# Performance work log

Hardware: AMD Instinct MI355X
Metric: run time of the kernel (lower is better)

## Reference

```python
import jax, jax.numpy as jnp
from jax import lax
import numpy as np

K = 7  # deformable conv kernel size
DN = ('NHWC', 'HWIO', 'NHWC')


def pad_zeros_2d(x, f=2):
    # zero-stuffing upsample by factor f in H and W (PadZeros2D(num_zeros=(2,2)))
    B, H, W, C = x.shape
    out = jnp.zeros((B, H * f, W * f, C), x.dtype)
    return out.at[:, ::f, ::f, :].set(x)


def bilinear_sample(x, pos):
    # x: [B,H,W,C]; pos: [B,H,W,KK,2] float (y,x) -> [B,H,W,KK,C]; out-of-bounds -> 0
    B, H, W, C = x.shape
    y, xx = pos[..., 0], pos[..., 1]
    y0 = jnp.floor(y)
    x0 = jnp.floor(xx)
    wy1 = y - y0
    wx1 = xx - x0
    b = jnp.arange(B)[:, None, None, None]

    def gather(yi, xi):
        valid = (yi >= 0) & (yi <= H - 1) & (xi >= 0) & (xi <= W - 1)
        yc = jnp.clip(yi, 0, H - 1).astype(jnp.int32)
        xc = jnp.clip(xi, 0, W - 1).astype(jnp.int32)
        return x[b, yc, xc] * valid[..., None].astype(x.dtype)

    return (gather(y0, x0) * ((1 - wy1) * (1 - wx1))[..., None]
            + gather(y0, x0 + 1) * ((1 - wy1) * wx1)[..., None]
            + gather(y0 + 1, x0) * (wy1 * (1 - wx1))[..., None]
            + gather(y0 + 1, x0 + 1) * (wy1 * wx1)[..., None])


def deform_conv2d(x, off_w, off_b, w, b):
    # deformable conv v1: offsets predicted by a same-padded KxK conv,
    # bilinear sampling at (base + kernel offset + learned offset), then accumulate.
    B, H, W, C = x.shape
    F = w.shape[-1]
    off = lax.conv_general_dilated(x, off_w, (1, 1), 'SAME', dimension_numbers=DN) + off_b
    off = off.reshape(B, H, W, K * K, 2)
    ki, kj = jnp.meshgrid(jnp.arange(K) - K // 2, jnp.arange(K) - K // 2, indexing='ij')
    kpos = jnp.stack([ki.ravel(), kj.ravel()], -1).astype(x.dtype)  # [49,2]
    base = jnp.stack(jnp.meshgrid(jnp.arange(H), jnp.arange(W), indexing='ij'), -1).astype(x.dtype)  # [H,W,2]
    pos = base[None, :, :, None, :] + kpos[None, None, None] + off  # [B,H,W,49,2]
    samp = bilinear_sample(x, pos)  # [B,H,W,49,C]
    return jnp.einsum('bhwkc,kcf->bhwf', samp, w.reshape(K * K, C, F)) + b


def setup_inputs() -> dict:
    key = jax.random.key(0)
    ks = jax.random.split(key, 20)
    latent, in_shape, chan = 128, (8, 16, 1024), 1
    D = int(np.prod(in_shape))
    filt = [in_shape[-1], 64, 32, 16, chan]

    def conv_w(k, cin, cout):
        return jax.random.normal(k, (K, K, cin, cout), jnp.float32) / np.sqrt(K * K * cin)

    inp = {
        'z_in': jax.random.normal(ks[0], (2, latent), jnp.float32),
        'dense_w': jax.random.normal(ks[1], (latent, D), jnp.float32) / np.sqrt(latent),
        'dense_b': jnp.zeros((D,), jnp.float32),
    }
    for i in range(4):
        cin, cout = filt[i], filt[i + 1]
        inp[f'ow{i+1}'] = conv_w(ks[2 + 4 * i], cin, 2 * K * K) * 0.01  # small offsets
        inp[f'ob{i+1}'] = jnp.zeros((2 * K * K,), jnp.float32)
        inp[f'w{i+1}'] = conv_w(ks[3 + 4 * i], cin, cout)
        inp[f'b{i+1}'] = jnp.zeros((cout,), jnp.float32)
    return inp


def reference(z_in, dense_w, dense_b, ow1, ob1, w1, b1, ow2, ob2, w2, b2,
              ow3, ob3, w3, b3, ow4, ob4, w4, b4):
    B = z_in.shape[0]
    x = jax.nn.relu((z_in @ dense_w + dense_b).reshape(B, 8, 16, 1024))
    x = jax.nn.relu(deform_conv2d(pad_zeros_2d(x), ow1, ob1, w1, b1))  # [B,16,32,64]
    x = jax.nn.relu(deform_conv2d(pad_zeros_2d(x), ow2, ob2, w2, b2))  # [B,32,64,32]
    x = jax.nn.relu(deform_conv2d(pad_zeros_2d(x), ow3, ob3, w3, b3))  # [B,64,128,16]
    x = deform_conv2d(pad_zeros_2d(x), ow4, ob4, w4, b4)               # [B,128,256,1]
    return x  # activation is linear
```

## Files before the change

kernel.cpp:

```cpp
#include <hip/hip_runtime.h>
#include <hip/hip_bf16.h>

#define K49 49

typedef short bf16x8 __attribute__((ext_vector_type(8)));
typedef float f32x4 __attribute__((ext_vector_type(4)));

__device__ __forceinline__ short f2bf(float x) {
    __hip_bfloat16 h = __float2bfloat16(x);
    return __builtin_bit_cast(short, h);
}
__device__ __forceinline__ float bf2f(short s) {
    unsigned u = ((unsigned)(unsigned short)s) << 16;
    return __builtin_bit_cast(float, u);
}

__device__ __forceinline__ void d_pack_ow1(
    const int gid, const float* __restrict__ OW, short* __restrict__ OWbf)
{
    const int ni = gid & 15;
    int t = gid >> 4;
    const int kg = t & 3;  t >>= 2;
    const int kb = t & 31; t >>= 5;
    const int nt = t % 7;
    const int d  = t / 7;
    const int oc = nt * 16 + ni;
    short h[8];
    if (oc < 98) {
        const int c0 = kb * 32 + kg * 8;
        #pragma unroll
        for (int j = 0; j < 8; ++j)
            h[j] = f2bf(OW[((size_t)d * 1024 + c0 + j) * 98 + oc]);
    } else {
        #pragma unroll
        for (int j = 0; j < 8; ++j) h[j] = 0;
    }
    *(bf16x8*)(OWbf + (size_t)gid * 8) = *(bf16x8*)h;
}

template<int C, int F>
__device__ __forceinline__ void d_pack_w(
    const int gid, const float* __restrict__ Wt, short* __restrict__ Wf)
{
    constexpr int KB = C / 32;
    constexpr int NT = F / 16;
    constexpr int PLANE = 49 * NT * KB * 4 * 16 * 8;
    const int ni = gid & 15;
    int t = gid >> 4;
    const int kg = t & 3; t >>= 2;
    const int kb = t % KB; t /= KB;
    const int nt = t % NT;
    const int d  = t / NT;
    const int f = nt * 16 + ni;
    const int c0 = kb * 32 + kg * 8;
    short hi[8], lo[8];
    #pragma unroll
    for (int j = 0; j < 8; ++j) {
        const float v = Wt[((size_t)d * C + c0 + j) * F + f];
        hi[j] = f2bf(v);
        lo[j] = f2bf(v - bf2f(hi[j]));
    }
    *(bf16x8*)(Wf + (size_t)gid * 8) = *(bf16x8*)hi;
    *(bf16x8*)(Wf + PLANE + (size_t)gid * 8) = *(bf16x8*)lo;
}

template<int C>
__device__ __forceinline__ void d_pack_owf(
    const int gid, const float* __restrict__ OW, short* __restrict__ OWf)
{
    const int j = gid & 7;
    int t = gid >> 3;
    const int fi = t & 63; t >>= 6;
    const int nt = t % 7;
    const int kbg = t / 7;
    const int ni = fi & 15, kg = fi >> 4;

    int cum1, cum2, cum3;
    if (C == 64)      { cum1 = 18; cum2 = 42; cum3 = 66; }
    else if (C == 32) { cum1 = 9;  cum2 = 21; cum3 = 33; }
    else              { cum1 = 5;  cum2 = 11; cum3 = 17; }
    int cls, kb0;
    if (kbg < cum1)      { cls = 0; kb0 = 0; }
    else if (kbg < cum2) { cls = 1; kb0 = cum1; }
    else if (kbg < cum3) { cls = 2; kb0 = cum2; }
    else                 { cls = 3; kb0 = cum3; }
    const int kbl = kbg - kb0;
    const int pi = cls >> 1, rho = cls & 1;
    const int NRc = pi ? 4 : 3, NCc = rho ? 4 : 3;
    const int T = NRc * NCc;

    const int k = kbl * 32 + kg * 8 + j;
    const int tl = k / C, c = k - tl * C;
    const int oc = nt * 16 + ni;
    float v = 0.f;
    if (tl < T && oc < 98) {
        const int iy = tl / NCc, ix = tl - iy * NCc;
        const int d = (1 - pi + 2 * iy) * 7 + (1 - rho + 2 * ix);
        v = OW[((size_t)d * C + c) * 98 + oc];
    }
    OWf[gid] = f2bf(v);
}

__global__ __launch_bounds__(256) void k_prep(
    const float* __restrict__ z, const float* __restrict__ Wd,
    const float* __restrict__ bd, short* __restrict__ Xf,
    const float* __restrict__ ow1, const float* __restrict__ w1,
    const float* __restrict__ ow2, const float* __restrict__ w2,
    const float* __restrict__ ow3, const float* __restrict__ w3,
    const float* __restrict__ ow4,
    short* OWbf, short* W1f, short* OWf2, short* W2f,
    short* OWf3, short* W3f, short* OWf4)
{
    const int bid0 = blockIdx.x;
    const int tid = threadIdx.x;
    __shared__ float zs[256];
    if (bid0 < 512) {
        const int D = 131072;
        zs[tid] = z[tid];
        __syncthreads();
        const int n = bid0 * 256 + tid;
        const float bb = bd[n];
        float a0 = bb, a1 = bb;
        #pragma unroll 8
        for (int kk = 0; kk < 128; ++kk) {
            const float w = Wd[kk * D + n];
            a0 = fmaf(zs[kk], w, a0);
            a1 = fmaf(zs[128 + kk], w, a1);
        }
        a0 = fmaxf(a0, 0.f);
        a1 = fmaxf(a1, 0.f);
        const int c = n & 1023;
        const int m0 = n >> 10;
        const int kb = c >> 5, kg = (c >> 3) & 3, j = c & 7;
        const size_t base = ((size_t)kb * 4 + kg) * 16 * 8 + j;
        {
            const size_t dst = ((size_t)(m0 >> 4) * 2048) * 8 + base + (size_t)(m0 & 15) * 8;
            const short h = f2bf(a0);
            Xf[dst] = h;
            Xf[262144 + dst] = f2bf(a0 - bf2f(h));
        }
        {
            const int m1 = m0 + 128;
            const size_t dst = ((size_t)(m1 >> 4) * 2048) * 8 + base + (size_t)(m1 & 15) * 8;
            const short h = f2bf(a1);
            Xf[dst] = h;
            Xf[262144 + dst] = f2bf(a1 - bf2f(h));
        }
        return;
    }
    const int bid = bid0 - 512;
    if (bid < 2744)      d_pack_ow1((bid) * 256 + tid, ow1, OWbf);
    else if (bid < 4312) d_pack_w<1024, 64>((bid - 2744) * 256 + tid, w1, W1f);
    else if (bid < 5684) d_pack_owf<64>((bid - 4312) * 256 + tid, ow2, OWf2);
    else if (bid < 5733) d_pack_w<64, 32>((bid - 5684) * 256 + tid, w2, W2f);
    else if (bid < 6419) d_pack_owf<32>((bid - 5733) * 256 + tid, ow3, OWf3);
    else if (bid < 6432) { const int g = (bid - 6419) * 256 + tid; if (g < 3136) d_pack_w<32, 16>(g, w3, W3f); }
    else                 d_pack_owf<16>((bid - 6432) * 256 + tid, ow4, OWf4);
}

__global__ __launch_bounds__(256) void k_gemms1(
    const short* __restrict__ Xf, const short* __restrict__ OWbf,
    const short* __restrict__ W1f,
    float* __restrict__ Zp, float* __restrict__ Y1)
{
    const int tid = threadIdx.x;
    const int wv = tid >> 6;
    const int l  = tid & 63;
    const int l15 = l & 15, l4 = l >> 4;

    const int wid = blockIdx.x + 4 * (blockIdx.y + 98 * blockIdx.z);
    const int work = (wid & 7) * 196 + (wid >> 3);
    const int x    = work & 3;
    const int rest = work >> 2;
    const int ks   = rest / 98;
    const int by   = rest - ks * 98;

    const int mtile = x * 4 + wv;
    const int kb0 = ks * 8;

    const bf16x8* Ah = (const bf16x8*)Xf + (size_t)mtile * 2048 + l4 * 16 + l15;
    const bf16x8* Al = Ah + 32768;
    const int m0 = mtile * 16 + l4 * 4;

    if (by < 49) {
        const int d = by;
        const bf16x8* Bb = (const bf16x8*)OWbf + (size_t)d * 7 * 2048 + l4 * 16 + l15;
        f32x4 acc[7];
        #pragma unroll
        for (int nt = 0; nt < 7; ++nt) acc[nt] = (f32x4){0.f, 0.f, 0.f, 0.f};
        #pragma unroll
        for (int i = 0; i < 8; ++i) {
            const int kb = kb0 + i;
            const bf16x8 ah = Ah[kb * 64];
            const bf16x8 al = Al[kb * 64];
            #pragma unroll
            for (int nt = 0; nt < 7; ++nt) {
                const bf16x8 b = Bb[(size_t)nt * 2048 + kb * 64];
                acc[nt] = __builtin_amdgcn_mfma_f32_16x16x32_bf16(ah, b, acc[nt], 0, 0, 0);
                acc[nt] = __builtin_amdgcn_mfma_f32_16x16x32_bf16(al, b, acc[nt], 0, 0, 0);
            }
        }
        float* Zo = Zp + (size_t)ks * 1229312;
        #pragma unroll
        for (int nt = 0; nt < 7; ++nt) {
            const int oc = nt * 16 + l15;
            if (oc < 98) {
                #pragma unroll
                for (int r = 0; r < 4; ++r)
                    Zo[((size_t)d * 256 + m0 + r) * 98 + oc] = acc[nt][r];
            }
        }
    } else {
        const int d = by - 49;
        const bf16x8* Bh = (const bf16x8*)W1f + (size_t)d * 4 * 2048 + l4 * 16 + l15;
        const bf16x8* Bl = Bh + 401408;
        f32x4 acc[4];
        #pragma unroll
        for (int nt = 0; nt < 4; ++nt) acc[nt] = (f32x4){0.f, 0.f, 0.f, 0.f};
        #pragma unroll
        for (int i = 0; i < 8; ++i) {
            const int kb = kb0 + i;
            const bf16x8 ah = Ah[kb * 64];
            const bf16x8 al = Al[kb * 64];
            #pragma unroll
            for (int nt = 0; nt < 4; ++nt) {
                const bf16x8 bh = Bh[nt * 2048 + kb * 64];
                const bf16x8 bl = Bl[nt * 2048 + kb * 64];
                acc[nt] = __builtin_amdgcn_mfma_f32_16x16x32_bf16(ah, bh, acc[nt], 0, 0, 0);
                acc[nt] = __builtin_amdgcn_mfma_f32_16x16x32_bf16(ah, bl, acc[nt], 0, 0, 0);
                acc[nt] = __builtin_amdgcn_mfma_f32_16x16x32_bf16(al, bh, acc[nt], 0, 0, 0);
            }
        }
        float* Yo = Y1 + (size_t)ks * 802816;
        #pragma unroll
        for (int nt = 0; nt < 4; ++nt) {
            const int f = nt * 16 + l15;
            #pragma unroll
            for (int r = 0; r < 4; ++r)
                Yo[((size_t)d * 256 + m0 + r) * 64 + f] = acc[nt][r];
        }
    }
}

__device__ __forceinline__ void d_bilin(
    const float accy, const float accx, const int hp, const int wp,
    const int b, const int k, const int H, const int W, const int Hp, const int Wp,
    float& s_out, int& src_out)
{
    const float y = (float)(hp + (k / 7) - 3) + accy;
    const float x = (float)(wp + (k % 7) - 3) + accx;
    const float fy0 = floorf(y), fx0 = floorf(x);
    const int iy0 = (int)fy0, ix0 = (int)fx0;
    const float wy1 = y - fy0, wx1 = x - fx0;
    int ye, xe; float wy, wx;
    if (iy0 & 1) { ye = iy0 + 1; wy = wy1; } else { ye = iy0; wy = 1.f - wy1; }
    if (ix0 & 1) { xe = ix0 + 1; wx = wx1; } else { xe = ix0; wx = 1.f - wx1; }
    float s = wy * wx;
    int src = 0;
    if (ye >= 0 && ye < Hp && xe >= 0 && xe < Wp)
        src = (b * H + (ye >> 1)) * W + (xe >> 1);
    else
        s = 0.f;
    s_out = s;
    src_out = src;
}

__global__ __launch_bounds__(256) void k_combine1(
    const float* __restrict__ Y, const float* __restrict__ Zp,
    const float* __restrict__ OB, const float* __restrict__ bias,
    short* __restrict__ xhi, short* __restrict__ xlo)
{
    __shared__ float ss[4][49];
    __shared__ int   isrc[4][49];
    const int tid = threadIdx.x;

    if (tid < 196) {
        const int p = tid / 49, k = tid - p * 49;
        const int pixg = blockIdx.x * 4 + p;
        const int b   = pixg >> 9;
        const int rem = pixg & 511;
        const int hp  = rem >> 5;
        const int wp  = rem & 31;
        float accy = OB[2 * k], accx = OB[2 * k + 1];
        const int di0 = (hp + 1) & 1, dj0 = (wp + 1) & 1;
        for (int di = di0; di < 7; di += 2) {
            const int yp = hp + di - 3;
            if ((unsigned)yp >= 16u) continue;
            const int ys = yp >> 1;
            for (int dj = dj0; dj < 7; dj += 2) {
                const int xp = wp + dj - 3;
                if ((unsigned)xp >= 32u) continue;
                const int xs = xp >> 1;
                const size_t o = ((size_t)((di * 7 + dj) * 256 + (b * 8 + ys) * 16 + xs)) * 98 + 2 * k;
                accy += (Zp[o] + Zp[o + 1229312]) + (Zp[o + 2458624] + Zp[o + 3687936]);
                accx += (Zp[o + 1] + Zp[o + 1229313]) + (Zp[o + 2458625] + Zp[o + 3687937]);
            }
        }
        d_bilin(accy, accx, hp, wp, b, k, 8, 16, 16, 32, ss[p][k], isrc[p][k]);
    }
    __syncthreads();

    const int f = tid & 63;
    const int p = tid >> 6;
    const int pixg = blockIdx.x * 4 + p;
    float acc = bias[f];
    #pragma unroll 7
    for (int k = 0; k < K49; ++k) {
        const size_t yo = ((size_t)k * 256 + isrc[p][k]) * 64 + f;
        const float yv = (Y[yo] + Y[yo + 802816]) + (Y[yo + 1605632] + Y[yo + 2408448]);
        acc = fmaf(ss[p][k], yv, acc);
    }
    const float v = fmaxf(acc, 0.f);
    const size_t o = (size_t)pixg * 64 + f;
    const short h = f2bf(v);
    xhi[o] = h;
    xlo[o] = f2bf(v - bf2f(h));
}

template<int C, int F>
__global__ __launch_bounds__(256) void k_gemms23(
    const short* __restrict__ Xbf, const short* __restrict__ OWf,
    const short* __restrict__ Wf,
    float* __restrict__ off, float* __restrict__ Y,
    const int H, const int W, const int Hp, const int Wp,
    const int M, const int nX)
{
    const int tid = threadIdx.x;
    const int wv = tid >> 6;
    const int l  = tid & 63;
    const int l15 = l & 15, l4 = l >> 4;
    const int by = blockIdx.y;

    if (by < 4) {
        const int cls = by;
        const int pi = cls >> 1, rho = cls & 1;
        const int NRc = pi ? 4 : 3, NCc = rho ? 4 : 3;
        const int T = NRc * NCc;
        int nkb, clsoff;
        if (C == 64) { nkb = T * 2; clsoff = cls == 0 ? 0 : cls == 1 ? 18 : cls == 2 ? 42 : 66; }
        else         { nkb = T;     clsoff = cls == 0 ? 0 : cls == 1 ? 9  : cls == 2 ? 21 : 33; }

        const int Wt16 = W >> 4;
        const int mt = blockIdx.x * 4 + wv;
        const int rloc = mt / Wt16, xt = mt - rloc * Wt16;
        const int b = rloc / H;
        const int ysp = rloc - b * H;

        f32x4 acc[7];
        #pragma unroll
        for (int nt = 0; nt < 7; ++nt) acc[nt] = (f32x4){0.f, 0.f, 0.f, 0.f};

        const bf16x8* Bbase = (const bf16x8*)OWf + ((size_t)clsoff * 7) * 64 + l4 * 16 + l15;

        for (int kb = 0; kb < nkb; ++kb) {
            int tl, c0;
            if (C == 64) { tl = kb >> 1; c0 = ((kb & 1) << 5) + l4 * 8; }
            else         { tl = kb;      c0 = l4 * 8; }
            int iy, ix;
            if (NCc == 4) { iy = tl >> 2; ix = tl & 3; }
            else          { iy = tl / 3;  ix = tl - iy * 3; }
            const int ys = ysp + iy - 1;
            const int xs = xt * 16 + l15 + ix - 1;
            bf16x8 ah = {0, 0, 0, 0, 0, 0, 0, 0};
            bf16x8 al = {0, 0, 0, 0, 0, 0, 0, 0};
            if ((unsigned)ys < (unsigned)H && (unsigned)xs < (unsigned)W) {
                const size_t a = ((size_t)(b * H + ys) * W + xs) * C + c0;
                ah = *(const bf16x8*)(Xbf + a);
                al = *(const bf16x8*)(Xbf + nX + a);
            }
            const bf16x8* Bb = Bbase + (size_t)kb * 7 * 64;
            #pragma unroll
            for (int nt = 0; nt < 7; ++nt) {
                const bf16x8 bf = Bb[nt * 64];
                acc[nt] = __builtin_amdgcn_mfma_f32_16x16x32_bf16(ah, bf, acc[nt], 0, 0, 0);
                acc[nt] = __builtin_amdgcn_mfma_f32_16x16x32_bf16(al, bf, acc[nt], 0, 0, 0);
            }
        }

        const int hp = 2 * ysp + pi;
        const int wpbase = (xt << 5) + rho;
        const int pixrow = (b * Hp + hp) * Wp + wpbase;
        #pragma unroll
        for (int nt = 0; nt < 7; ++nt) {
            const int oc = nt * 16 + l15;
            if (oc < 98) {
                #pragma unroll
                for (int r = 0; r < 4; ++r) {
                    const int m = l4 * 4 + r;
                    off[(size_t)(pixrow + 2 * m) * 98 + oc] = acc[nt][r];
                }
            }
        }
    } else {
        constexpr int KB = C / 32;
        constexpr int NT = F / 16;
        constexpr int PLANEFRAG = 49 * NT * KB * 64;
        const int d = by - 4;
        const int mtile = blockIdx.x * 4 + wv;
        const short* Arow = Xbf + (size_t)(mtile * 16 + l15) * C + l4 * 8;

        f32x4 acc[NT];
        #pragma unroll
        for (int nt = 0; nt < NT; ++nt) acc[nt] = (f32x4){0.f, 0.f, 0.f, 0.f};

        #pragma unroll
        for (int kb = 0; kb < KB; ++kb) {
            const bf16x8 ah = *(const bf16x8*)(Arow + kb * 32);
            const bf16x8 al = *(const bf16x8*)(Arow + nX + kb * 32);
            #pragma unroll
            for (int nt = 0; nt < NT; ++nt) {
                const size_t fi = ((size_t)(d * NT + nt) * KB + kb) * 64 + l4 * 16 + l15;
                const bf16x8 bh = ((const bf16x8*)Wf)[fi];
                const bf16x8 bl = ((const bf16x8*)Wf)[fi + PLANEFRAG];
                acc[nt] = __builtin_amdgcn_mfma_f32_16x16x32_bf16(ah, bh, acc[nt], 0, 0, 0);
                acc[nt] = __builtin_amdgcn_mfma_f32_16x16x32_bf16(ah, bl, acc[nt], 0, 0, 0);
                acc[nt] = __builtin_amdgcn_mfma_f32_16x16x32_bf16(al, bh, acc[nt], 0, 0, 0);
            }
        }

        const int m0 = mtile * 16 + l4 * 4;
        #pragma unroll
        for (int nt = 0; nt < NT; ++nt) {
            const int f = nt * 16 + l15;
            #pragma unroll
            for (int r = 0; r < 4; ++r)
                Y[((size_t)d * M + m0 + r) * F + f] = acc[nt][r];
        }
    }
}

template<int F, bool DO_Y4>
__global__ __launch_bounds__(256) void k_combine23(
    const float* __restrict__ Y, const float* __restrict__ off,
    const float* __restrict__ OB, const float* __restrict__ bias,
    short* __restrict__ xhi, short* __restrict__ xlo,
    const float* __restrict__ w4, float* __restrict__ Y4,
    const int npix, const int nsrc,
    const int H, const int W, const int Hp, const int Wp)
{
    constexpr int PPB = 256 / F;
    __shared__ float ss[PPB][49];
    __shared__ int   isrc[PPB][49];
    __shared__ float xv[DO_Y4 ? PPB : 1][DO_Y4 ? 17 : 1];
    __shared__ float w4s[DO_Y4 ? 784 : 1];
    const int tid = threadIdx.x;
    const int HWp = Hp * Wp;

    if (DO_Y4) {
        for (int t = tid; t < 784; t += 256) w4s[t] = w4[t];
    }
    for (int t = tid; t < PPB * 49; t += 256) {
        const int p = t / 49, k = t - p * 49;
        const int pixg = blockIdx.x * PPB + p;
        const float accy = OB[2 * k]     + off[(size_t)pixg * 98 + 2 * k];
        const float accx = OB[2 * k + 1] + off[(size_t)pixg * 98 + 2 * k + 1];
        const int b = pixg / HWp;
        const int rem = pixg - b * HWp;
        const int hp = rem / Wp;
        const int wp = rem - hp * Wp;
        d_bilin(accy, accx, hp, wp, b, k, H, W, Hp, Wp, ss[p][k], isrc[p][k]);
    }
    __syncthreads();

    const int f = tid % F;
    const int p2 = tid / F;
    const int pixg2 = blockIdx.x * PPB + p2;
    float acc = bias[f];
    #pragma unroll 7
    for (int k = 0; k < K49; ++k)
        acc = fmaf(ss[p2][k], Y[((size_t)k * nsrc + isrc[p2][k]) * F + f], acc);
    const float v = fmaxf(acc, 0.f);
    const size_t o = (size_t)pixg2 * F + f;
    const short h = f2bf(v);
    xhi[o] = h;
    xlo[o] = f2bf(v - bf2f(h));

    if (DO_Y4) {
        xv[p2][f] = v;
        __syncthreads();
        for (int t = tid; t < PPB * 49; t += 256) {
            const int p = t / 49, k = t - p * 49;
            float d = 0.f;
            #pragma unroll
            for (int f2 = 0; f2 < 16; ++f2)
                d = fmaf(xv[p][f2], w4s[k * 16 + f2], d);
            Y4[(size_t)k * npix + blockIdx.x * PPB + p] = d;
        }
    }
}

__global__ __launch_bounds__(256) void k_offmfma4(
    const short* __restrict__ Xbf, const short* __restrict__ OWf,
    float* __restrict__ off,
    const int H, const int W, const int Hp, const int Wp, const int nX)
{
    constexpr int C = 16;
    const int tid = threadIdx.x;
    const int wv = tid >> 6;
    const int l  = tid & 63;
    const int l15 = l & 15, l4 = l >> 4;
    const int cls = blockIdx.y;
    const int pi = cls >> 1, rho = cls & 1;
    const int NRc = pi ? 4 : 3, NCc = rho ? 4 : 3;
    const int T = NRc * NCc;
    const int nkb = (T + 1) >> 1;
    const int clsoff = cls == 0 ? 0 : cls == 1 ? 5 : cls == 2 ? 11 : 17;

    const int Wt16 = W >> 4;
    const int mt = blockIdx.x * 4 + wv;
    const int rloc = mt / Wt16, xt = mt - rloc * Wt16;
    const int b = rloc / H;
    const int ysp = rloc - b * H;

    f32x4 acc[7];
    #pragma unroll
    for (int nt = 0; nt < 7; ++nt) acc[nt] = (f32x4){0.f, 0.f, 0.f, 0.f};

    const bf16x8* Bbase = (const bf16x8*)OWf + ((size_t)clsoff * 7) * 64 + l4 * 16 + l15;

    for (int kb = 0; kb < nkb; ++kb) {
        int tl = kb * 2 + (l4 >> 1);
        const int c0 = (l4 & 1) * 8;
        if (tl >= T) tl = T - 1;
        int iy, ix;
        if (NCc == 4) { iy = tl >> 2; ix = tl & 3; }
        else          { iy = tl / 3;  ix = tl - iy * 3; }
        const int ys = ysp + iy - 1;
        const int xs = xt * 16 + l15 + ix - 1;
        bf16x8 ah = {0, 0, 0, 0, 0, 0, 0, 0};
        bf16x8 al = {0, 0, 0, 0, 0, 0, 0, 0};
        if ((unsigned)ys < (unsigned)H && (unsigned)xs < (unsigned)W) {
            const size_t a = ((size_t)(b * H + ys) * W + xs) * C + c0;
            ah = *(const bf16x8*)(Xbf + a);
            al = *(const bf16x8*)(Xbf + nX + a);
        }
        const bf16x8* Bb = Bbase + (size_t)kb * 7 * 64;
        #pragma unroll
        for (int nt = 0; nt < 7; ++nt) {
            const bf16x8 bf = Bb[nt * 64];
            acc[nt] = __builtin_amdgcn_mfma_f32_16x16x32_bf16(ah, bf, acc[nt], 0, 0, 0);
            acc[nt] = __builtin_amdgcn_mfma_f32_16x16x32_bf16(al, bf, acc[nt], 0, 0, 0);
        }
    }

    const int hp = 2 * ysp + pi;
    const int wpbase = (xt << 5) + rho;
    const int pixrow = (b * Hp + hp) * Wp + wpbase;
    #pragma unroll
    for (int nt = 0; nt < 7; ++nt) {
        const int oc = nt * 16 + l15;
        if (oc < 98) {
            #pragma unroll
            for (int r = 0; r < 4; ++r) {
                const int m = l4 * 4 + r;
                off[(size_t)(pixrow + 2 * m) * 98 + oc] = acc[nt][r];
            }
        }
    }
}

__global__ __launch_bounds__(256) void k_dconv_f1_y(
    const float* __restrict__ Y4,
    const float* __restrict__ part,
    const float* __restrict__ OB,
    const float* __restrict__ bias, float* __restrict__ out,
    const int H, const int W, const int Hp, const int Wp,
    const int nsrc)
{
    __shared__ float OBs[98];
    const int tid = threadIdx.x;
    if (tid < 98) OBs[tid] = OB[tid];
    __syncthreads();

    const int pixL = blockIdx.x * 64 + (tid >> 2);
    const int tq = tid & 3;
    const int t0 = (tq == 0) ? 0 : 13 + (tq - 1) * 12;
    const int t1 = t0 + ((tq == 0) ? 13 : 12);

    const int HWp = Hp * Wp;
    const int b = pixL / HWp;
    const int rem = pixL - b * HWp;
    const int hp = rem / Wp;
    const int wp = rem - hp * Wp;

    float acc = 0.f;
    for (int k = t0; k < t1; ++k) {
        const float offy = part[(size_t)pixL * 98 + 2 * k]     + OBs[2 * k];
        const float offx = part[(size_t)pixL * 98 + 2 * k + 1] + OBs[2 * k + 1];
        float s; int src;
        d_bilin(offy, offx, hp, wp, b, k, H, W, Hp, Wp, s, src);
        acc = fmaf(s, Y4[(size_t)k * nsrc + src], acc);
    }
    acc += __shfl_xor(acc, 1);
    acc += __shfl_xor(acc, 2);
    if (tq == 0) out[pixL] = acc + bias[0];
}

extern "C" void kernel_launch(void* const* d_in, const int* in_sizes, int n_in,
                              void* d_out, int out_size, void* d_ws, size_t ws_size,
                              hipStream_t stream) {
    const float* z   = (const float*)d_in[0];
    const float* dw  = (const float*)d_in[1];
    const float* db  = (const float*)d_in[2];
    const float* ow1 = (const float*)d_in[3];
    const float* ob1 = (const float*)d_in[4];
    const float* w1  = (const float*)d_in[5];
    const float* b1  = (const float*)d_in[6];
    const float* ow2 = (const float*)d_in[7];
    const float* ob2 = (const float*)d_in[8];
    const float* w2  = (const float*)d_in[9];
    const float* b2  = (const float*)d_in[10];
    const float* ow3 = (const float*)d_in[11];
    const float* ob3 = (const float*)d_in[12];
    const float* w3  = (const float*)d_in[13];
    const float* b3  = (const float*)d_in[14];
    const float* ow4 = (const float*)d_in[15];
    const float* ob4 = (const float*)d_in[16];
    const float* w4  = (const float*)d_in[17];
    const float* b4  = (const float*)d_in[18];

    float* ws   = (float*)d_ws;
    short* Xf   = (short*)ws;
    float* Zp   = ws + 262144;
    float* Y1   = Zp + 4917248;
    float* Y2   = Y1 + 3211264;
    float* Y3   = Y2 + 1605632;
    float* Y4   = Y3 + 3211264;
    short* Xbf1 = (short*)(Y4 + 802816);
    short* Xbf2 = Xbf1 + 131072;
    short* Xbf3 = Xbf2 + 262144;
    float* off2 = (float*)(Xbf3 + 524288);
    float* off3 = off2 + 401408;
    float* off4 = off3 + 1605632;
    short* OWbf = (short*)(off4 + 6422528);
    short* W1f  = OWbf + 5619712;
    short* OWf2 = W1f + 6422528;
    short* W2f  = OWf2 + 351232;
    short* OWf3 = W2f + 200704;
    short* W3f  = OWf3 + 175616;
    short* OWf4 = W3f + 50176;

    float* out = (float*)d_out;

    k_prep<<<7294, 256, 0, stream>>>(z, dw, db, Xf, ow1, w1, ow2, w2, ow3, w3, ow4,
                                     OWbf, W1f, OWf2, W2f, OWf3, W3f, OWf4);

    k_gemms1<<<dim3(4, 98, 4), 256, 0, stream>>>(Xf, OWbf, W1f, Zp, Y1);

    k_combine1<<<256, 256, 0, stream>>>(Y1, Zp, ob1, b1, Xbf1, Xbf1 + 65536);

    k_gemms23<64, 32><<<dim3(16, 53), 256, 0, stream>>>(
        Xbf1, OWf2, W2f, off2, Y2, 16, 32, 32, 64, 1024, 65536);

    k_combine23<32, false><<<512, 256, 0, stream>>>(
        Y2, off2, ob2, b2, Xbf2, Xbf2 + 131072, nullptr, nullptr, 4096, 1024, 16, 32, 32, 64);

    k_gemms23<32, 16><<<dim3(64, 53), 256, 0, stream>>>(
        Xbf2, OWf3, W3f, off3, Y3, 32, 64, 64, 128, 4096, 131072);

    k_combine23<16, true><<<1024, 256, 0, stream>>>(
        Y3, off3, ob3, b3, Xbf3, Xbf3 + 262144, w4, Y4, 16384, 4096, 32, 64, 64, 128);

    k_offmfma4<<<dim3(256, 4), 256, 0, stream>>>(Xbf3, OWf4, off4, 64, 128, 128, 256, 262144);

    k_dconv_f1_y<<<1024, 256, 0, stream>>>(Y4, off4, ob4, b4, out, 64, 128, 128, 256, 16384);
}
```

Baseline: 153.8 us.

## Fuse stage-4 offset MFMA conv with bilinear sampling via shared memory

Merges the stage-4 offset-prediction MFMA kernel and the single-channel deformable sampling kernel into one kernel. Offsets for the block's 64 pixels are staged in LDS rather than written to and re-read from a large global buffer, which also removes one kernel launch. The cost is about 25KB of LDS per block, which may lower occupancy, and hardcoded layer dimensions.

```diff
diff --git a/kernel.cpp b/kernel.cpp
--- a/kernel.cpp
+++ b/kernel.cpp
@@ -489,12 +489,16 @@
     }
 }
 
-__global__ __launch_bounds__(256) void k_offmfma4(
+__global__ __launch_bounds__(256) void k_stage4(
     const short* __restrict__ Xbf, const short* __restrict__ OWf,
-    float* __restrict__ off,
-    const int H, const int W, const int Hp, const int Wp, const int nX)
-{
-    constexpr int C = 16;
+    const float* __restrict__ Y4,
+    const float* __restrict__ OB, const float* __restrict__ bias,
+    float* __restrict__ out, const int nX)
+{
+    constexpr int C = 16, H = 64, W = 128, Hp = 128, Wp = 256;
+    __shared__ float offs[64][98];
+    __shared__ float OBs[98];
+
     const int tid = threadIdx.x;
     const int wv = tid >> 6;
     const int l  = tid & 63;
@@ -506,9 +510,10 @@
     const int nkb = (T + 1) >> 1;
     const int clsoff = cls == 0 ? 0 : cls == 1 ? 5 : cls == 2 ? 11 : 17;
 
-    const int Wt16 = W >> 4;
+    if (tid < 98) OBs[tid] = OB[tid];
+
     const int mt = blockIdx.x * 4 + wv;
-    const int rloc = mt / Wt16, xt = mt - rloc * Wt16;
+    const int rloc = mt >> 3, xt = mt & 7;
     const int b = rloc / H;
     const int ysp = rloc - b * H;
 
@@ -543,57 +548,43 @@
         }
     }
 
-    const int hp = 2 * ysp + pi;
-    const int wpbase = (xt << 5) + rho;
-    const int pixrow = (b * Hp + hp) * Wp + wpbase;
     #pragma unroll
     for (int nt = 0; nt < 7; ++nt) {
         const int oc = nt * 16 + l15;
         if (oc < 98) {
             #pragma unroll
-            for (int r = 0; r < 4; ++r) {
-                const int m = l4 * 4 + r;
-                off[(size_t)(pixrow + 2 * m) * 98 + oc] = acc[nt][r];
-            }
-        }
-    }
-}
-
-__global__ __launch_bounds__(256) void k_dconv_f1_y(
-    const float* __restrict__ Y4,
-    const float* __restrict__ part,
-    const float* __restrict__ OB,
-    const float* __restrict__ bias, float* __restrict__ out,
-    const int H, const int W, const int Hp, const int Wp,
-    const int nsrc)
-{
-    __shared__ float OBs[98];
-    const int tid = threadIdx.x;
-    if (tid < 98) OBs[tid] = OB[tid];
+            for (int r = 0; r < 4; ++r)
+                offs[wv * 16 + l4 * 4 + r][oc] = acc[nt][r];
+        }
+    }
     __syncthreads();
 
-    const int pixL = blockIdx.x * 64 + (tid >> 2);
+    const int p  = tid >> 2;
     const int tq = tid & 3;
     const int t0 = (tq == 0) ? 0 : 13 + (tq - 1) * 12;
     const int t1 = t0 + ((tq == 0) ? 13 : 12);
 
-    const int HWp = Hp * Wp;
-    const int b = pixL / HWp;
-    const int rem = pixL - b * HWp;
-    const int hp = rem / Wp;
-    const int wp = rem - hp * Wp;
-
-    float acc = 0.f;
+    const int wv_p = p >> 4;
+    const int m_p  = p & 15;
+    const int mt_p = blockIdx.x * 4 + wv_p;
+    const int rloc_p = mt_p >> 3, xt_p = mt_p & 7;
+    const int b_p = rloc_p / H;
+    const int ysp_p = rloc_p - b_p * H;
+    const int hp = 2 * ysp_p + pi;
+    const int wp = (xt_p << 5) + rho + 2 * m_p;
+    const int pixg = (b_p * Hp + hp) * Wp + wp;
+
+    float acc2 = 0.f;
     for (int k = t0; k < t1; ++k) {
-        const float offy = part[(size_t)pixL * 98 + 2 * k]     + OBs[2 * k];
-        const float offx = part[(size_t)pixL * 98 + 2 * k + 1] + OBs[2 * k + 1];
+        const float offy = offs[p][2 * k]     + OBs[2 * k];
+        const float offx = offs[p][2 * k + 1] + OBs[2 * k + 1];
         float s; int src;
-        d_bilin(offy, offx, hp, wp, b, k, H, W, Hp, Wp, s, src);
-        acc = fmaf(s, Y4[(size_t)k * nsrc + src], acc);
-    }
-    acc += __shfl_xor(acc, 1);
-    acc += __shfl_xor(acc, 2);
-    if (tq == 0) out[pixL] = acc + bias[0];
+        d_bilin(offy, offx, hp, wp, b_p, k, H, W, Hp, Wp, s, src);
+        acc2 = fmaf(s, Y4[(size_t)k * 16384 + src], acc2);
+    }
+    acc2 += __shfl_xor(acc2, 1);
+    acc2 += __shfl_xor(acc2, 2);
+    if (tq == 0) out[pixg] = acc2 + bias[0];
 }
 
 extern "C" void kernel_launch(void* const* d_in, const int* in_sizes, int n_in,
@@ -631,8 +622,7 @@
     short* Xbf3 = Xbf2 + 262144;
     float* off2 = (float*)(Xbf3 + 524288);
     float* off3 = off2 + 401408;
-    float* off4 = off3 + 1605632;
-    short* OWbf = (short*)(off4 + 6422528);
+    short* OWbf = (short*)(off3 + 1605632);
     short* W1f  = OWbf + 5619712;
     short* OWf2 = W1f + 6422528;
     short* W2f  = OWf2 + 351232;
@@ -661,7 +651,5 @@
     k_combine23<16, true><<<1024, 256, 0, stream>>>(
         Y3, off3, ob3, b3, Xbf3, Xbf3 + 262144, w4, Y4, 16384, 4096, 32, 64, 64, 128);
 
-    k_offmfma4<<<dim3(256, 4), 256, 0, stream>>>(Xbf3, OWf4, off4, 64, 128, 128, 256, 262144);
-
-    k_dconv_f1_y<<<1024, 256, 0, stream>>>(Y4, off4, ob4, b4, out, 64, 128, 128, 256, 16384);
-}
+    k_stage4<<<dim3(256, 4), 256, 0, stream>>>(Xbf3, OWf4, Y4, ob4, b4, out, 262144);
+}
```

New measurement: 137.2 us. 10.8% less time.
